# Optimization experiments

Measured on AMD Instinct MI355X. Metric: run time of the kernel, lower is better.

The kernel has to match this reference:

```python
import jax, jax.numpy as jnp
import numpy as np

H = 5  # hidden size of both LSTMs

def _lstm_layer(x, Wih, Whh, bih, bhh):
    """x: [B,T,I] -> hs: [B,T,H]. PyTorch gate order i,f,g,o; zero init state."""
    B, T, _ = x.shape
    # precompute input contribution for all timesteps: [T,B,4H]
    xg = (jnp.einsum('bti,gi->btg', x, Wih) + bih + bhh).transpose(1, 0, 2)
    def step(carry, xg_t):
        h, c = carry
        g = xg_t + h @ Whh.T
        i, f, gg, o = jnp.split(g, 4, axis=-1)
        c = jax.nn.sigmoid(f) * c + jax.nn.sigmoid(i) * jnp.tanh(gg)
        h = jax.nn.sigmoid(o) * jnp.tanh(c)
        return (h, c), h
    h0 = jnp.zeros((B, H), x.dtype)
    (_, _), hs = jax.lax.scan(step, (h0, h0), xg)
    return hs.transpose(1, 0, 2)  # [B,T,H]

def setup_inputs() -> dict:
    key = jax.random.key(0)
    ks = jax.random.split(key, 32)
    B, T = 16384, 128
    def u(k, shape, fan):
        s = 1.0 / np.sqrt(fan)
        return jax.random.uniform(k, shape, jnp.float32, -s, s)
    inp = {
        'x1': jax.random.normal(ks[0], (B, T, 5), jnp.float32),
        'x2': jax.random.normal(ks[1], (B, T, 5), jnp.float32),
        # lstm1 (1 layer)
        'Wih1': u(ks[2], (4*H, 5), H), 'Whh1': u(ks[3], (4*H, H), H),
        'bih1': u(ks[4], (4*H,), H), 'bhh1': u(ks[5], (4*H,), H),
        # lstm2 layer 0
        'Wih2a': u(ks[6], (4*H, 5), H), 'Whh2a': u(ks[7], (4*H, H), H),
        'bih2a': u(ks[8], (4*H,), H), 'bhh2a': u(ks[9], (4*H,), H),
        # lstm2 layer 1
        'Wih2b': u(ks[10], (4*H, H), H), 'Whh2b': u(ks[11], (4*H, H), H),
        'bih2b': u(ks[12], (4*H,), H), 'bhh2b': u(ks[13], (4*H,), H),
        # FC stack 20->32->32->16->16->5
        'W1': u(ks[14], (32, 20), 20), 'b1': u(ks[15], (32,), 20),
        'W2': u(ks[16], (32, 32), 32), 'b2': u(ks[17], (32,), 32),
        'W3': u(ks[18], (16, 32), 32), 'b3': u(ks[19], (16,), 32),
        'W4': u(ks[20], (16, 16), 16), 'b4': u(ks[21], (16,), 16),
        'W5': u(ks[22], (5, 16), 16), 'b5': u(ks[23], (5,), 16),
    }
    return inp

def reference(x1, x2, Wih1, Whh1, bih1, bhh1, Wih2a, Whh2a, bih2a, bhh2a,
              Wih2b, Whh2b, bih2b, bhh2b, W1, b1, W2, b2, W3, b3, W4, b4, W5, b5):
    out1 = _lstm_layer(x1, Wih1, Whh1, bih1, bhh1)[:, -1, :]            # [B,5]
    h2 = _lstm_layer(x2, Wih2a, Whh2a, bih2a, bhh2a)                    # [B,T,5]
    out2 = _lstm_layer(h2, Wih2b, Whh2b, bih2b, bhh2b)[:, -1, :]        # [B,5]
    out = jnp.concatenate([x1[:, -1, :], x2[:, -1, :], out1, out2], axis=1)  # [B,20]
    out = jax.nn.relu(out @ W1.T + b1)
    out = jax.nn.relu(out @ W2.T + b2)
    out = jax.nn.relu(out @ W3.T + b3)
    out = jax.nn.relu(out @ W4.T + b4)
    return out @ W5.T + b5  # [B,5]
```

## Files before the change

kernel.cpp:

```cpp
#include <hip/hip_runtime.h>

#define DEV __device__ __forceinline__

DEV float fexp2(float x) { return __builtin_amdgcn_exp2f(x); }
DEV float frcp(float x) { return __builtin_amdgcn_rcpf(x); }

template <int S>
DEV float qbcast(float x) {
#if __has_builtin(__builtin_amdgcn_update_dpp)
  int i = __float_as_int(x);
  i = __builtin_amdgcn_update_dpp(0, i, S * 0x55, 0xF, 0xF, true);
  return __int_as_float(i);
#else
  return __shfl(x, S, 4);
#endif
}

struct Cell {
  float wih[5][5];
  float whh[5][5];
  float b[5];
};

DEV void load_cell(Cell& W, const float* __restrict__ Wih,
                   const float* __restrict__ Whh, const float* __restrict__ bih,
                   const float* __restrict__ bhh, int s) {
#pragma unroll
  for (int j = 0; j < 5; ++j) {
    int r = 5 * s + j;
#pragma unroll
    for (int k = 0; k < 5; ++k) {
      W.wih[j][k] = Wih[r * 5 + k];
      W.whh[j][k] = Whh[r * 5 + k];
    }
    W.b[j] = bih[r] + bhh[r];
  }
}

DEV void cell_step(const Cell& W, float kexp, float m2, float a2,
                   const float x[5], float h[5], float c[5]) {
  float a[5];
#pragma unroll
  for (int j = 0; j < 5; ++j) {
    float acc = W.b[j];
#pragma unroll
    for (int k = 0; k < 5; ++k) acc = fmaf(W.wih[j][k], x[k], acc);
#pragma unroll
    for (int k = 0; k < 5; ++k) acc = fmaf(W.whh[j][k], h[k], acc);
    float e = fexp2(acc * kexp);
    float r = frcp(1.0f + e);
    a[j] = fmaf(m2, r, a2);
  }
#pragma unroll
  for (int j = 0; j < 5; ++j) {
    float I = qbcast<0>(a[j]);
    float F = qbcast<1>(a[j]);
    float G = qbcast<2>(a[j]);
    float O = qbcast<3>(a[j]);
    float cj = fmaf(F, c[j], I * G);
    c[j] = cj;
    float e2 = fexp2(cj * -2.885390082f);
    float tc = fmaf(2.0f, frcp(1.0f + e2), -1.0f);
    h[j] = O * tc;
  }
}

DEV void lds_copy(float* dst, const float* __restrict__ src, int n, int tid) {
  for (int i = tid; i < n; i += 256) dst[i] = src[i];
}

__global__ __launch_bounds__(256, 1) void rnn_fused_kernel(
    const float* __restrict__ x1, const float* __restrict__ x2,
    const float* __restrict__ Wih1, const float* __restrict__ Whh1,
    const float* __restrict__ bih1, const float* __restrict__ bhh1,
    const float* __restrict__ Wih2a, const float* __restrict__ Whh2a,
    const float* __restrict__ bih2a, const float* __restrict__ bhh2a,
    const float* __restrict__ Wih2b, const float* __restrict__ Whh2b,
    const float* __restrict__ bih2b, const float* __restrict__ bhh2b,
    const float* __restrict__ W1, const float* __restrict__ b1,
    const float* __restrict__ W2, const float* __restrict__ b2,
    const float* __restrict__ W3, const float* __restrict__ b3,
    const float* __restrict__ W4, const float* __restrict__ b4,
    const float* __restrict__ W5, const float* __restrict__ b5,
    float* __restrict__ out, int B) {
  __shared__ __align__(16) float sFC[2613];
  {
    int tl = threadIdx.x;
    lds_copy(sFC + 0, W1, 640, tl);
    lds_copy(sFC + 640, b1, 32, tl);
    lds_copy(sFC + 672, W2, 1024, tl);
    lds_copy(sFC + 1696, b2, 32, tl);
    lds_copy(sFC + 1728, W3, 512, tl);
    lds_copy(sFC + 2240, b3, 16, tl);
    lds_copy(sFC + 2256, W4, 256, tl);
    lds_copy(sFC + 2512, b4, 16, tl);
    lds_copy(sFC + 2528, W5, 80, tl);
    lds_copy(sFC + 2608, b5, 5, tl);
  }
  __syncthreads();

  int tid = blockIdx.x * 256 + threadIdx.x;
  int e = tid >> 2;
  int s = tid & 3;
  if (e >= B) return;

  Cell WA, WB, WC;
  load_cell(WA, Wih1, Whh1, bih1, bhh1, s);
  load_cell(WB, Wih2a, Whh2a, bih2a, bhh2a, s);
  load_cell(WC, Wih2b, Whh2b, bih2b, bhh2b, s);

  const float kexp = (s == 2) ? -2.885390082f : -1.442695041f;
  const float m2 = (s == 2) ? 2.0f : 1.0f;
  const float a2 = (s == 2) ? -1.0f : 0.0f;

  const float* px1 = x1 + (size_t)e * 640;
  const float* px2 = x2 + (size_t)e * 640;

  float h1[5], c1[5], h2a[5], c2a[5], h2b[5], c2b[5];
#pragma unroll
  for (int k = 0; k < 5; ++k) {
    h1[k] = c1[k] = h2a[k] = c2a[k] = h2b[k] = c2b[k] = 0.0f;
  }

  float xa[5], xb[5];
#pragma unroll
  for (int k = 0; k < 5; ++k) {
    xa[k] = px1[k];
    xb[k] = px2[k];
  }

  for (int t = 0; t < 128; ++t) {
    int tn = (t < 127) ? t + 1 : 127;
    float nxa[5], nxb[5];
#pragma unroll
    for (int k = 0; k < 5; ++k) {
      nxa[k] = px1[tn * 5 + k];
      nxb[k] = px2[tn * 5 + k];
    }
    cell_step(WA, kexp, m2, a2, xa, h1, c1);
    cell_step(WB, kexp, m2, a2, xb, h2a, c2a);
    cell_step(WC, kexp, m2, a2, h2a, h2b, c2b);
#pragma unroll
    for (int k = 0; k < 5; ++k) {
      xa[k] = nxa[k];
      xb[k] = nxb[k];
    }
  }

  float in0[20];
#pragma unroll
  for (int k = 0; k < 5; ++k) {
    in0[k] = xa[k];
    in0[5 + k] = xb[k];
    in0[10 + k] = h1[k];
    in0[15 + k] = h2b[k];
  }
  float v1[32];
#pragma unroll
  for (int n = 0; n < 32; ++n) {
    float acc = sFC[640 + n];
#pragma unroll
    for (int k = 0; k < 20; ++k) acc = fmaf(sFC[n * 20 + k], in0[k], acc);
    v1[n] = fmaxf(acc, 0.0f);
  }
  float v2[32];
#pragma unroll
  for (int n = 0; n < 32; ++n) {
    float acc = sFC[1696 + n];
#pragma unroll
    for (int k = 0; k < 32; ++k) acc = fmaf(sFC[672 + n * 32 + k], v1[k], acc);
    v2[n] = fmaxf(acc, 0.0f);
  }
  float v3[16];
#pragma unroll
  for (int n = 0; n < 16; ++n) {
    float acc = sFC[2240 + n];
#pragma unroll
    for (int k = 0; k < 32; ++k) acc = fmaf(sFC[1728 + n * 32 + k], v2[k], acc);
    v3[n] = fmaxf(acc, 0.0f);
  }
  float v4[16];
#pragma unroll
  for (int n = 0; n < 16; ++n) {
    float acc = sFC[2512 + n];
#pragma unroll
    for (int k = 0; k < 16; ++k) acc = fmaf(sFC[2256 + n * 16 + k], v3[k], acc);
    v4[n] = fmaxf(acc, 0.0f);
  }
  if (s == 0) {
#pragma unroll
    for (int n = 0; n < 5; ++n) {
      float acc = sFC[2608 + n];
#pragma unroll
      for (int k = 0; k < 16; ++k)
        acc = fmaf(sFC[2528 + n * 16 + k], v4[k], acc);
      out[(size_t)e * 5 + n] = acc;
    }
  }
}

extern "C" void kernel_launch(void* const* d_in, const int* in_sizes, int n_in,
                              void* d_out, int out_size, void* d_ws,
                              size_t ws_size, hipStream_t stream) {
  const float* x1 = (const float*)d_in[0];
  const float* x2 = (const float*)d_in[1];
  const float* Wih1 = (const float*)d_in[2];
  const float* Whh1 = (const float*)d_in[3];
  const float* bih1 = (const float*)d_in[4];
  const float* bhh1 = (const float*)d_in[5];
  const float* Wih2a = (const float*)d_in[6];
  const float* Whh2a = (const float*)d_in[7];
  const float* bih2a = (const float*)d_in[8];
  const float* bhh2a = (const float*)d_in[9];
  const float* Wih2b = (const float*)d_in[10];
  const float* Whh2b = (const float*)d_in[11];
  const float* bih2b = (const float*)d_in[12];
  const float* bhh2b = (const float*)d_in[13];
  const float* W1 = (const float*)d_in[14];
  const float* b1 = (const float*)d_in[15];
  const float* W2 = (const float*)d_in[16];
  const float* b2 = (const float*)d_in[17];
  const float* W3 = (const float*)d_in[18];
  const float* b3 = (const float*)d_in[19];
  const float* W4 = (const float*)d_in[20];
  const float* b4 = (const float*)d_in[21];
  const float* W5 = (const float*)d_in[22];
  const float* b5 = (const float*)d_in[23];

  int B = in_sizes[0] / 640;
  int threads = B * 4;
  int blocks = (threads + 255) / 256;

  rnn_fused_kernel<<<blocks, 256, 0, stream>>>(
      x1, x2, Wih1, Whh1, bih1, bhh1, Wih2a, Whh2a, bih2a, bhh2a, Wih2b, Whh2b,
      bih2b, bhh2b, W1, b1, W2, b2, W3, b3, W4, b4, W5, b5, (float*)d_out, B);
}
```

Baseline: 253.1 us.

## Compute LSTM gate matmuls with split-fp16 MFMA and split FC into separate kernel

Replaces the per-lane scalar FMA LSTM cells with a wave-per-16-elements design: gate pre-activations are computed by 16x16x32 fp16 MFMAs using hi/lo split weights and inputs to retain near-fp32 accuracy. Inputs and hidden states are staged in LDS as split halves each timestep, and gate results are exchanged via LDS. The FC stack moves to a second kernel that reads final hidden states from scratch buffers. This trades the scalar FMA work for matrix-core throughput but adds LDS traffic, extra MFMAs for the split precision, and a second launch.

```diff
diff --git a/kernel.cpp b/kernel.cpp
--- a/kernel.cpp
+++ b/kernel.cpp
@@ -1,75 +1,102 @@
 #include <hip/hip_runtime.h>
 
-#define DEV __device__ __forceinline__
-
-DEV float fexp2(float x) { return __builtin_amdgcn_exp2f(x); }
-DEV float frcp(float x) { return __builtin_amdgcn_rcpf(x); }
-
-template <int S>
-DEV float qbcast(float x) {
-#if __has_builtin(__builtin_amdgcn_update_dpp)
-  int i = __float_as_int(x);
-  i = __builtin_amdgcn_update_dpp(0, i, S * 0x55, 0xF, 0xF, true);
-  return __int_as_float(i);
-#else
-  return __shfl(x, S, 4);
-#endif
-}
-
-struct Cell {
-  float wih[5][5];
-  float whh[5][5];
-  float b[5];
+typedef _Float16 half8 __attribute__((ext_vector_type(8)));
+typedef float float4v __attribute__((ext_vector_type(4)));
+typedef int int4v __attribute__((ext_vector_type(4)));
+
+#define KSIG (-1.442695041f)
+#define KTANH (-2.885390082f)
+
+__device__ __forceinline__ float fexp2(float x) { return __builtin_amdgcn_exp2f(x); }
+__device__ __forceinline__ float frcp(float x) { return __builtin_amdgcn_rcpf(x); }
+
+union H8 {
+  half8 v;
+  _Float16 a[8];
 };
 
-DEV void load_cell(Cell& W, const float* __restrict__ Wih,
-                   const float* __restrict__ Whh, const float* __restrict__ bih,
-                   const float* __restrict__ bhh, int s) {
-#pragma unroll
-  for (int j = 0; j < 5; ++j) {
-    int r = 5 * s + j;
-#pragma unroll
-    for (int k = 0; k < 5; ++k) {
-      W.wih[j][k] = Wih[r * 5 + k];
-      W.whh[j][k] = Whh[r * 5 + k];
+struct CellW {
+  half8 bh[2], bl[2];
+  float4v bias[2];
+};
+
+__device__ __forceinline__ void load_cellW(CellW& cw, int lane,
+                                           const float* __restrict__ Wih,
+                                           const float* __restrict__ Whh,
+                                           const float* __restrict__ bih,
+                                           const float* __restrict__ bhh) {
+  int n0 = lane & 15, q = lane >> 4;
+#pragma unroll
+  for (int tl = 0; tl < 2; ++tl) {
+    int n = tl * 16 + n0;
+    float kx = (n >= 10 && n < 15) ? KTANH : KSIG;
+    float bv = (n < 20) ? kx * (bih[n] + bhh[n]) : 0.f;
+    cw.bias[tl] = (float4v){bv, bv, bv, bv};
+    H8 hh, hl;
+#pragma unroll
+    for (int j = 0; j < 8; ++j) {
+      int k = q * 8 + j;
+      float w = 0.f;
+      if (n < 20 && k < 10) w = kx * (k < 5 ? Wih[n * 5 + k] : Whh[n * 5 + (k - 5)]);
+      _Float16 wh = (_Float16)w;
+      hh.a[j] = wh;
+      hl.a[j] = (_Float16)(w - (float)wh);
     }
-    W.b[j] = bih[r] + bhh[r];
-  }
-}
-
-DEV void cell_step(const Cell& W, float kexp, float m2, float a2,
-                   const float x[5], float h[5], float c[5]) {
-  float a[5];
-#pragma unroll
-  for (int j = 0; j < 5; ++j) {
-    float acc = W.b[j];
-#pragma unroll
-    for (int k = 0; k < 5; ++k) acc = fmaf(W.wih[j][k], x[k], acc);
-#pragma unroll
-    for (int k = 0; k < 5; ++k) acc = fmaf(W.whh[j][k], h[k], acc);
-    float e = fexp2(acc * kexp);
-    float r = frcp(1.0f + e);
-    a[j] = fmaf(m2, r, a2);
-  }
-#pragma unroll
-  for (int j = 0; j < 5; ++j) {
-    float I = qbcast<0>(a[j]);
-    float F = qbcast<1>(a[j]);
-    float G = qbcast<2>(a[j]);
-    float O = qbcast<3>(a[j]);
-    float cj = fmaf(F, c[j], I * G);
-    c[j] = cj;
-    float e2 = fexp2(cj * -2.885390082f);
-    float tc = fmaf(2.0f, frcp(1.0f + e2), -1.0f);
-    h[j] = O * tc;
-  }
-}
-
-DEV void lds_copy(float* dst, const float* __restrict__ src, int n, int tid) {
-  for (int i = tid; i < n; i += 256) dst[i] = src[i];
-}
-
-__global__ __launch_bounds__(256, 1) void rnn_fused_kernel(
+    cw.bh[tl] = hh.v;
+    cw.bl[tl] = hl.v;
+  }
+}
+
+__device__ __forceinline__ void wr_hl(char* base, int byteoff, float v) {
+  _Float16 h = (_Float16)v;
+  *(_Float16*)(base + byteoff) = h;
+  *(_Float16*)(base + 1024 + byteoff) = (_Float16)(v - (float)h);
+}
+
+#define CELL_LDS 4160
+
+__device__ __forceinline__ void cell_iter(
+    char* base, const CellW& cw, int l, int q, int n0, float m2_0, float a2_0,
+    int gr0, int gr1, int hw0, int hw1, bool p1v, float* cst, float* hout,
+    char* fwd_base, int aw0, int aw1) {
+  half8 ah = *(const half8*)(base + l * 16);
+  half8 al = *(const half8*)(base + 1024 + l * 16);
+
+  float4v acc0 = __builtin_amdgcn_mfma_f32_16x16x32_f16(ah, cw.bh[0], cw.bias[0], 0, 0, 0);
+  acc0 = __builtin_amdgcn_mfma_f32_16x16x32_f16(al, cw.bh[0], acc0, 0, 0, 0);
+  acc0 = __builtin_amdgcn_mfma_f32_16x16x32_f16(ah, cw.bl[0], acc0, 0, 0, 0);
+  float4v acc1 = __builtin_amdgcn_mfma_f32_16x16x32_f16(ah, cw.bh[1], cw.bias[1], 0, 0, 0);
+  acc1 = __builtin_amdgcn_mfma_f32_16x16x32_f16(al, cw.bh[1], acc1, 0, 0, 0);
+  acc1 = __builtin_amdgcn_mfma_f32_16x16x32_f16(ah, cw.bl[1], acc1, 0, 0, 0);
+
+  float* sG = (float*)(base + 2048);
+#pragma unroll
+  for (int r = 0; r < 4; ++r) {
+    int row = q * 4 + r;
+    float g0 = fmaf(m2_0, frcp(1.f + fexp2(acc0[r])), a2_0);
+    sG[row * 33 + n0] = g0;
+    float g1 = frcp(1.f + fexp2(acc1[r]));
+    sG[row * 33 + 16 + n0] = g1;
+  }
+
+#pragma unroll
+  for (int p = 0; p < 2; ++p) {
+    int gr = p ? gr1 : gr0;
+    float I = sG[gr], F = sG[gr + 5], G = sG[gr + 10], O = sG[gr + 15];
+    float c = fmaf(F, cst[p], I * G);
+    cst[p] = c;
+    float th = fmaf(2.f, frcp(1.f + fexp2(KTANH * c)), -1.f);
+    float h = O * th;
+    hout[p] = h;
+    bool w = p ? p1v : true;
+    if (w) {
+      wr_hl(base, p ? hw1 : hw0, h);
+      if (fwd_base) wr_hl(fwd_base, p ? aw1 : aw0, h);
+    }
+  }
+}
+
+__global__ __launch_bounds__(64) void rnn_mfma_kernel(
     const float* __restrict__ x1, const float* __restrict__ x2,
     const float* __restrict__ Wih1, const float* __restrict__ Whh1,
     const float* __restrict__ bih1, const float* __restrict__ bhh1,
@@ -77,125 +104,143 @@
     const float* __restrict__ bih2a, const float* __restrict__ bhh2a,
     const float* __restrict__ Wih2b, const float* __restrict__ Whh2b,
     const float* __restrict__ bih2b, const float* __restrict__ bhh2b,
+    float* __restrict__ wsh1, float* __restrict__ wsh2, int B) {
+  __shared__ __align__(16) unsigned char sMem[3 * CELL_LDS];
+  char* base0 = (char*)sMem;
+  char* base1 = (char*)sMem + CELL_LDS;
+  char* base2 = (char*)sMem + 2 * CELL_LDS;
+
+  const int l = threadIdx.x;
+  const int g = blockIdx.x;
+  const int n0 = l & 15, q = l >> 4;
+
+  CellW w0, w1, w2;
+  load_cellW(w0, l, Wih1, Whh1, bih1, bhh1);
+  load_cellW(w1, l, Wih2a, Whh2a, bih2a, bhh2a);
+  load_cellW(w2, l, Wih2b, Whh2b, bih2b, bhh2b);
+
+  int4v z = (int4v){0, 0, 0, 0};
+  *(int4v*)(base0 + l * 16) = z;
+  *(int4v*)(base0 + 1024 + l * 16) = z;
+  *(int4v*)(base1 + l * 16) = z;
+  *(int4v*)(base1 + 1024 + l * 16) = z;
+  *(int4v*)(base2 + l * 16) = z;
+  *(int4v*)(base2 + 1024 + l * 16) = z;
+
+  const float m2_0 = (n0 >= 10 && n0 < 15) ? 2.f : 1.f;
+  const float a2_0 = (n0 >= 10 && n0 < 15) ? -1.f : 0.f;
+
+  const int e0 = (l * 205) >> 10, j0 = l - e0 * 5;
+  const int s1i = 64 + n0;
+  const int e1 = (s1i * 205) >> 10, j1 = s1i - e1 * 5;
+  const bool p1v = (l < 16);
+
+  const float* px1_0 = x1 + (size_t)(g * 16 + e0) * 640 + j0;
+  const float* px1_1 = x1 + (size_t)(g * 16 + e1) * 640 + j1;
+  const float* px2_0 = x2 + (size_t)(g * 16 + e0) * 640 + j0;
+  const float* px2_1 = x2 + (size_t)(g * 16 + e1) * 640 + j1;
+
+  const int xw0 = e0 * 16 + j0 * 2;
+  const int xw1 = e1 * 16 + j1 * 2;
+  const int k0 = 5 + j0;
+  const int hw0 = (k0 < 8) ? (e0 * 16 + k0 * 2) : ((16 + e0) * 16 + (k0 - 8) * 2);
+  const int k1 = 5 + j1;
+  const int hw1 = (k1 < 8) ? (e1 * 16 + k1 * 2) : ((16 + e1) * 16 + (k1 - 8) * 2);
+
+  const int gr0 = e0 * 33 + j0;
+  const int gr1 = e1 * 33 + j1;
+
+  float c0[2] = {0.f, 0.f}, c1s[2] = {0.f, 0.f}, c2[2] = {0.f, 0.f};
+  float h1o[2] = {0.f, 0.f}, h2ao[2] = {0.f, 0.f}, h2bo[2] = {0.f, 0.f};
+
+  float xa0 = px1_0[0], xa1 = px1_1[0];
+  float xb0 = px2_0[0], xb1 = px2_1[0];
+
+  for (int t = 0; t < 128; ++t) {
+    wr_hl(base0, xw0, xa0);
+    if (p1v) wr_hl(base0, xw1, xa1);
+    wr_hl(base1, xw0, xb0);
+    if (p1v) wr_hl(base1, xw1, xb1);
+
+    int tn = (t < 127) ? t + 1 : 127;
+    xa0 = px1_0[tn * 5];
+    xa1 = px1_1[tn * 5];
+    xb0 = px2_0[tn * 5];
+    xb1 = px2_1[tn * 5];
+
+    cell_iter(base0, w0, l, q, n0, m2_0, a2_0, gr0, gr1, hw0, hw1, p1v, c0,
+              h1o, nullptr, 0, 0);
+    cell_iter(base1, w1, l, q, n0, m2_0, a2_0, gr0, gr1, hw0, hw1, p1v, c1s,
+              h2ao, base2, xw0, xw1);
+    cell_iter(base2, w2, l, q, n0, m2_0, a2_0, gr0, gr1, hw0, hw1, p1v, c2,
+              h2bo, nullptr, 0, 0);
+  }
+
+  wsh1[(size_t)g * 80 + l] = h1o[0];
+  wsh2[(size_t)g * 80 + l] = h2bo[0];
+  if (p1v) {
+    wsh1[(size_t)g * 80 + 64 + l] = h1o[1];
+    wsh2[(size_t)g * 80 + 64 + l] = h2bo[1];
+  }
+}
+
+__global__ __launch_bounds__(64) void fc_kernel(
+    const float* __restrict__ x1, const float* __restrict__ x2,
+    const float* __restrict__ wsh1, const float* __restrict__ wsh2,
     const float* __restrict__ W1, const float* __restrict__ b1,
     const float* __restrict__ W2, const float* __restrict__ b2,
     const float* __restrict__ W3, const float* __restrict__ b3,
     const float* __restrict__ W4, const float* __restrict__ b4,
     const float* __restrict__ W5, const float* __restrict__ b5,
     float* __restrict__ out, int B) {
-  __shared__ __align__(16) float sFC[2613];
-  {
-    int tl = threadIdx.x;
-    lds_copy(sFC + 0, W1, 640, tl);
-    lds_copy(sFC + 640, b1, 32, tl);
-    lds_copy(sFC + 672, W2, 1024, tl);
-    lds_copy(sFC + 1696, b2, 32, tl);
-    lds_copy(sFC + 1728, W3, 512, tl);
-    lds_copy(sFC + 2240, b3, 16, tl);
-    lds_copy(sFC + 2256, W4, 256, tl);
-    lds_copy(sFC + 2512, b4, 16, tl);
-    lds_copy(sFC + 2528, W5, 80, tl);
-    lds_copy(sFC + 2608, b5, 5, tl);
-  }
-  __syncthreads();
-
-  int tid = blockIdx.x * 256 + threadIdx.x;
-  int e = tid >> 2;
-  int s = tid & 3;
+  int e = blockIdx.x * 64 + threadIdx.x;
   if (e >= B) return;
-
-  Cell WA, WB, WC;
-  load_cell(WA, Wih1, Whh1, bih1, bhh1, s);
-  load_cell(WB, Wih2a, Whh2a, bih2a, bhh2a, s);
-  load_cell(WC, Wih2b, Whh2b, bih2b, bhh2b, s);
-
-  const float kexp = (s == 2) ? -2.885390082f : -1.442695041f;
-  const float m2 = (s == 2) ? 2.0f : 1.0f;
-  const float a2 = (s == 2) ? -1.0f : 0.0f;
-
-  const float* px1 = x1 + (size_t)e * 640;
-  const float* px2 = x2 + (size_t)e * 640;
-
-  float h1[5], c1[5], h2a[5], c2a[5], h2b[5], c2b[5];
+  float in0[20];
 #pragma unroll
   for (int k = 0; k < 5; ++k) {
-    h1[k] = c1[k] = h2a[k] = c2a[k] = h2b[k] = c2b[k] = 0.0f;
-  }
-
-  float xa[5], xb[5];
-#pragma unroll
-  for (int k = 0; k < 5; ++k) {
-    xa[k] = px1[k];
-    xb[k] = px2[k];
-  }
-
-  for (int t = 0; t < 128; ++t) {
-    int tn = (t < 127) ? t + 1 : 127;
-    float nxa[5], nxb[5];
-#pragma unroll
-    for (int k = 0; k < 5; ++k) {
-      nxa[k] = px1[tn * 5 + k];
-      nxb[k] = px2[tn * 5 + k];
-    }
-    cell_step(WA, kexp, m2, a2, xa, h1, c1);
-    cell_step(WB, kexp, m2, a2, xb, h2a, c2a);
-    cell_step(WC, kexp, m2, a2, h2a, h2b, c2b);
-#pragma unroll
-    for (int k = 0; k < 5; ++k) {
-      xa[k] = nxa[k];
-      xb[k] = nxb[k];
-    }
-  }
-
-  float in0[20];
-#pragma unroll
-  for (int k = 0; k < 5; ++k) {
-    in0[k] = xa[k];
-    in0[5 + k] = xb[k];
-    in0[10 + k] = h1[k];
-    in0[15 + k] = h2b[k];
+    in0[k] = x1[(size_t)e * 640 + 635 + k];
+    in0[5 + k] = x2[(size_t)e * 640 + 635 + k];
+    in0[10 + k] = wsh1[(size_t)e * 5 + k];
+    in0[15 + k] = wsh2[(size_t)e * 5 + k];
   }
   float v1[32];
 #pragma unroll
   for (int n = 0; n < 32; ++n) {
-    float acc = sFC[640 + n];
-#pragma unroll
-    for (int k = 0; k < 20; ++k) acc = fmaf(sFC[n * 20 + k], in0[k], acc);
-    v1[n] = fmaxf(acc, 0.0f);
+    float acc = b1[n];
+#pragma unroll
+    for (int k = 0; k < 20; ++k) acc = fmaf(W1[n * 20 + k], in0[k], acc);
+    v1[n] = fmaxf(acc, 0.f);
   }
   float v2[32];
 #pragma unroll
   for (int n = 0; n < 32; ++n) {
-    float acc = sFC[1696 + n];
-#pragma unroll
-    for (int k = 0; k < 32; ++k) acc = fmaf(sFC[672 + n * 32 + k], v1[k], acc);
-    v2[n] = fmaxf(acc, 0.0f);
+    float acc = b2[n];
+#pragma unroll
+    for (int k = 0; k < 32; ++k) acc = fmaf(W2[n * 32 + k], v1[k], acc);
+    v2[n] = fmaxf(acc, 0.f);
   }
   float v3[16];
 #pragma unroll
   for (int n = 0; n < 16; ++n) {
-    float acc = sFC[2240 + n];
-#pragma unroll
-    for (int k = 0; k < 32; ++k) acc = fmaf(sFC[1728 + n * 32 + k], v2[k], acc);
-    v3[n] = fmaxf(acc, 0.0f);
+    float acc = b3[n];
+#pragma unroll
+    for (int k = 0; k < 32; ++k) acc = fmaf(W3[n * 32 + k], v2[k], acc);
+    v3[n] = fmaxf(acc, 0.f);
   }
   float v4[16];
 #pragma unroll
   for (int n = 0; n < 16; ++n) {
-    float acc = sFC[2512 + n];
-#pragma unroll
-    for (int k = 0; k < 16; ++k) acc = fmaf(sFC[2256 + n * 16 + k], v3[k], acc);
-    v4[n] = fmaxf(acc, 0.0f);
-  }
-  if (s == 0) {
-#pragma unroll
-    for (int n = 0; n < 5; ++n) {
-      float acc = sFC[2608 + n];
-#pragma unroll
-      for (int k = 0; k < 16; ++k)
-        acc = fmaf(sFC[2528 + n * 16 + k], v4[k], acc);
-      out[(size_t)e * 5 + n] = acc;
-    }
+    float acc = b4[n];
+#pragma unroll
+    for (int k = 0; k < 16; ++k) acc = fmaf(W4[n * 16 + k], v3[k], acc);
+    v4[n] = fmaxf(acc, 0.f);
+  }
+#pragma unroll
+  for (int n = 0; n < 5; ++n) {
+    float acc = b5[n];
+#pragma unroll
+    for (int k = 0; k < 16; ++k) acc = fmaf(W5[n * 16 + k], v4[k], acc);
+    out[(size_t)e * 5 + n] = acc;
   }
 }
 
@@ -228,10 +273,13 @@
   const float* b5 = (const float*)d_in[23];
 
   int B = in_sizes[0] / 640;
-  int threads = B * 4;
-  int blocks = (threads + 255) / 256;
-
-  rnn_fused_kernel<<<blocks, 256, 0, stream>>>(
-      x1, x2, Wih1, Whh1, bih1, bhh1, Wih2a, Whh2a, bih2a, bhh2a, Wih2b, Whh2b,
-      bih2b, bhh2b, W1, b1, W2, b2, W3, b3, W4, b4, W5, b5, (float*)d_out, B);
-}
+  float* wsh1 = (float*)d_out;
+  float* wsh2 = (float*)d_ws;
+
+  rnn_mfma_kernel<<<B / 16, 64, 0, stream>>>(x1, x2, Wih1, Whh1, bih1, bhh1,
+                                             Wih2a, Whh2a, bih2a, bhh2a, Wih2b,
+                                             Whh2b, bih2b, bhh2b, wsh1, wsh2, B);
+  fc_kernel<<<(B + 63) / 64, 64, 0, stream>>>(x1, x2, wsh1, wsh2, W1, b1, W2,
+                                              b2, W3, b3, W4, b4, W5, b5,
+                                              (float*)d_out, B);
+}
```

Result: slower. 343.6 us (+35.7%).
